# Kernel optimization log

Measured on AMD Instinct MI355X. Metric: run time of the kernel, lower is better.

The kernel has to match this reference:

```python
import jax, jax.numpy as jnp
import numpy as np

B, S, D, H = 2, 2048, 2048, 16
HD = D // H          # head_dim = 128
FF = 8192            # intermediate_size
LN_EPS = 1e-05
BIT_EPS = 1e-05


def _rope_tables(seq_len, head_dim):
    inv_freq = 1.0 / (10000.0 ** (np.arange(0, head_dim, 2, dtype=np.float64) / head_dim))
    ang = np.arange(seq_len, dtype=np.float64)[:, None] * inv_freq[None, :]  # [S, HD/2]
    ang = np.concatenate([ang, ang], axis=-1)  # [S, HD]
    return jnp.asarray(np.cos(ang), jnp.float32), jnp.asarray(np.sin(ang), jnp.float32)


def setup_inputs() -> dict:
    key = jax.random.key(0)
    ks = jax.random.split(key, 9)
    hidden_states = jax.random.normal(ks[0], (B, S, D), jnp.float32)
    # causal additive mask [1, S, S]
    causal = jnp.tril(jnp.ones((S, S), bool))
    attention_mask = jnp.where(causal, 0.0, -1e9)[None].astype(jnp.float32)
    cos, sin = _rope_tables(S, HD)
    w = lambda k, o, i: jax.random.normal(k, (o, i), jnp.float32) * 0.02
    return {
        'hidden_states': hidden_states,
        'attention_mask': attention_mask,
        'cos': cos, 'sin': sin,
        'wq': w(ks[1], D, D), 'wk': w(ks[2], D, D),
        'wv': w(ks[3], D, D), 'wo': w(ks[4], D, D),
        'wg': w(ks[5], FF, D), 'wu': w(ks[6], FF, D), 'wd': w(ks[7], D, FF),
        'ln1_w': jnp.ones((D,), jnp.float32),
        'ln2_w': jnp.ones((D,), jnp.float32),
    }


def bitlinear(x, w):
    # ternarize: clamp(round(w / (mean|w| + eps)), -1, 1); int8 cast in torch
    # breaks grad through the ternary values -> stop_gradient here.
    scale = jnp.mean(jnp.abs(w))
    tern = jax.lax.stop_gradient(jnp.clip(jnp.round(w / (scale + BIT_EPS)), -1.0, 1.0))
    # dequant = ternary * mean|w|, then standard linear (x @ W^T)
    return jnp.einsum('bsi,oi->bso', x, tern * scale)


def rmsnorm(x, w, eps=LN_EPS):
    var = jnp.mean(jnp.square(x.astype(jnp.float32)), axis=-1, keepdims=True)
    return w * (x * jax.lax.rsqrt(var + eps))


def rotate_half(x):
    x1, x2 = jnp.split(x, 2, axis=-1)
    return jnp.concatenate([-x2, x1], axis=-1)


def apply_rope(q, k, cos, sin):
    # q, k: [B, S, D] -> per-head rope -> back to [B, S, D]
    qh = q.reshape(B, S, H, HD)
    kh = k.reshape(B, S, H, HD)
    c = cos[None, :, None, :]
    s = sin[None, :, None, :]
    qe = qh * c + rotate_half(qh) * s
    ke = kh * c + rotate_half(kh) * s
    return qe.reshape(B, S, D), ke.reshape(B, S, D)


def reference(hidden_states, attention_mask, cos, sin,
              wq, wk, wv, wo, wg, wu, wd, ln1_w, ln2_w):
    residual = hidden_states
    # --- attention block ---
    x = rmsnorm(hidden_states, ln1_w)
    q = bitlinear(x, wq)
    k = bitlinear(x, wk)
    v = bitlinear(x, wv)
    q, k = apply_rope(q, k, cos, sin)
    # NOTE: scores over FULL hidden dim (no head split), scaled by sqrt(head_dim),
    # exactly as in the original module.
    scores = jnp.einsum('bsd,btd->bst', q, k) / jnp.sqrt(jnp.float32(HD))
    scores = scores + attention_mask
    probs = jax.nn.softmax(scores, axis=-1)
    attn_out = jnp.einsum('bst,btd->bsd', probs, v)
    attn_out = bitlinear(attn_out, wo)
    h = residual + attn_out
    # --- MLP block ---
    residual = h
    y = rmsnorm(h, ln2_w)
    gated = bitlinear(y, wg) * bitlinear(y, wu)
    out = bitlinear(gated, wd)
    return residual + out
```

## Files before the change

kernel.cpp:

```cpp
#include <hip/hip_runtime.h>
#include <stdint.h>

#define DEV __device__ __forceinline__

typedef __attribute__((ext_vector_type(8))) short short8;
typedef __attribute__((ext_vector_type(8))) __bf16 bf16x8;
typedef __attribute__((ext_vector_type(4))) float f32x4;

DEV unsigned short f2bf(float f) {
  union { float f; unsigned int u; } v; v.f = f;
  unsigned int r = v.u + 0x7fffu + ((v.u >> 16) & 1u);
  return (unsigned short)(r >> 16);
}
DEV float bf2f(unsigned short h) {
  union { unsigned int u; float f; } v; v.u = ((unsigned int)h) << 16;
  return v.f;
}
DEV f32x4 mfma16(short8 a, short8 b, f32x4 c) {
  return __builtin_amdgcn_mfma_f32_16x16x32_bf16(
      __builtin_bit_cast(bf16x8, a), __builtin_bit_cast(bf16x8, b), c, 0, 0, 0);
}
DEV void gload_lds16(const void* g, void* lds) {
  __builtin_amdgcn_global_load_lds(
      (const __attribute__((address_space(1))) void*)g,
      (__attribute__((address_space(3))) void*)lds, 16, 0, 0);
}

struct MArgs {
  const float* src[7];
  unsigned short* dst[7];
  int n[7];
  int sidx[7];
};

__global__ __launch_bounds__(256) void absmean_partial_multi(
    MArgs a, float* __restrict__ partial) {
  const int m = blockIdx.y;
  const float4* w4 = (const float4*)a.src[m];
  const int n4 = a.n[m] >> 2;
  float s = 0.f;
  for (int i = blockIdx.x * 256 + threadIdx.x; i < n4; i += 1024 * 256) {
    float4 v = w4[i];
    s += fabsf(v.x) + fabsf(v.y) + fabsf(v.z) + fabsf(v.w);
  }
#pragma unroll
  for (int mm = 1; mm < 64; mm <<= 1) s += __shfl_xor(s, mm);
  __shared__ float red[4];
  if ((threadIdx.x & 63) == 0) red[threadIdx.x >> 6] = s;
  __syncthreads();
  if (threadIdx.x == 0)
    partial[m * 1024 + blockIdx.x] = red[0] + red[1] + red[2] + red[3];
}

__global__ __launch_bounds__(256) void absmean_final(
    const float* __restrict__ partial, float* __restrict__ scales) {
  __shared__ double red[256];
  const int m = blockIdx.x;
  double s = 0.0;
  for (int i = threadIdx.x; i < 1024; i += 256) s += (double)partial[m * 1024 + i];
  red[threadIdx.x] = s;
  __syncthreads();
  for (int t = 128; t > 0; t >>= 1) {
    if (threadIdx.x < t) red[threadIdx.x] += red[threadIdx.x + t];
    __syncthreads();
  }
  if (threadIdx.x == 0) {
    const long long cnt = (m < 4) ? 4194304ll : 16777216ll;
    scales[m] = (float)(red[0] / (double)cnt);
  }
}

__global__ __launch_bounds__(256) void quantize_multi(
    MArgs a, const float* __restrict__ scales) {
  const int m = blockIdx.y;
  const float sc = scales[a.sidx[m]];
  const float inv = 1.f / (sc + 1e-5f);
  const float4* src = (const float4*)a.src[m];
  ushort4* dst = (ushort4*)a.dst[m];
  const int n4 = a.n[m] >> 2;
  for (int i = blockIdx.x * 256 + threadIdx.x; i < n4; i += 2048 * 256) {
    float4 v = src[i];
    ushort4 o;
    o.x = f2bf(fminf(fmaxf(rintf(v.x * inv), -1.f), 1.f) * sc);
    o.y = f2bf(fminf(fmaxf(rintf(v.y * inv), -1.f), 1.f) * sc);
    o.z = f2bf(fminf(fmaxf(rintf(v.z * inv), -1.f), 1.f) * sc);
    o.w = f2bf(fminf(fmaxf(rintf(v.w * inv), -1.f), 1.f) * sc);
    dst[i] = o;
  }
}

__global__ __launch_bounds__(256) void rmsnorm_k(
    const float* __restrict__ x, const float* __restrict__ wt,
    unsigned short* __restrict__ out) {
  const long long t = blockIdx.x;
  const float* xr = x + t * 2048;
  const int i0 = threadIdx.x * 8;
  float4 a = *(const float4*)(xr + i0);
  float4 b = *(const float4*)(xr + i0 + 4);
  float ss = a.x * a.x + a.y * a.y + a.z * a.z + a.w * a.w +
             b.x * b.x + b.y * b.y + b.z * b.z + b.w * b.w;
#pragma unroll
  for (int m = 1; m < 64; m <<= 1) ss += __shfl_xor(ss, m);
  __shared__ float red[4];
  if ((threadIdx.x & 63) == 0) red[threadIdx.x >> 6] = ss;
  __syncthreads();
  float tot = red[0] + red[1] + red[2] + red[3];
  float rs = rsqrtf(tot * (1.f / 2048.f) + 1e-5f);
  float4 wa = *(const float4*)(wt + i0);
  float4 wb = *(const float4*)(wt + i0 + 4);
  ushort4 o1, o2;
  o1.x = f2bf(a.x * wa.x * rs); o1.y = f2bf(a.y * wa.y * rs);
  o1.z = f2bf(a.z * wa.z * rs); o1.w = f2bf(a.w * wa.w * rs);
  o2.x = f2bf(b.x * wb.x * rs); o2.y = f2bf(b.y * wb.y * rs);
  o2.z = f2bf(b.z * wb.z * rs); o2.w = f2bf(b.w * wb.w * rs);
  *(ushort4*)(out + t * 2048 + i0) = o1;
  *(ushort4*)(out + t * 2048 + i0 + 4) = o2;
}

__global__ __launch_bounds__(256) void rope_k(
    const unsigned short* __restrict__ qkv, const float* __restrict__ cosT,
    const float* __restrict__ sinT, unsigned short* __restrict__ qr,
    unsigned short* __restrict__ kr, unsigned short* __restrict__ vt) {
  const long long gid = (long long)blockIdx.x * 256 + threadIdx.x;
  const int t = (int)(gid >> 10);
  const int r = (int)(gid & 1023);
  const int h = r >> 6, d = r & 63;
  const int s = t & 2047, b = t >> 11;
  const unsigned short* row = qkv + (long long)t * 6144;
  const float c = cosT[s * 128 + d], sn = sinT[s * 128 + d];
  const int col = h * 128 + d;
  const float SC = 0.08838834764831845f;
  float q1 = bf2f(row[col]), q2 = bf2f(row[col + 64]);
  float k1 = bf2f(row[2048 + col]), k2 = bf2f(row[2048 + col + 64]);
  long long ob = (long long)t * 2048 + col;
  qr[ob] = f2bf((q1 * c - q2 * sn) * SC);
  qr[ob + 64] = f2bf((q2 * c + q1 * sn) * SC);
  kr[ob] = f2bf(k1 * c - k2 * sn);
  kr[ob + 64] = f2bf(k2 * c + k1 * sn);
  vt[((long long)b * 2048 + col) * 2048 + s] = row[4096 + col];
  vt[((long long)b * 2048 + col + 64) * 2048 + s] = row[4096 + col + 64];
}

__global__ __launch_bounds__(256) void softmax_causal(
    const float* __restrict__ scores, unsigned short* __restrict__ probs) {
  const int r = blockIdx.x;
  const int s = r & 2047;
  const float* src = scores + (long long)r * 2048;
  unsigned short* dst = probs + (long long)r * 2048;
  const int L = s + 1;
  const int j0 = threadIdx.x * 8;
  float4 a = *(const float4*)(src + j0);
  float4 b = *(const float4*)(src + j0 + 4);
  float v[8] = {a.x, a.y, a.z, a.w, b.x, b.y, b.z, b.w};
  float mx = -1e30f;
#pragma unroll
  for (int i = 0; i < 8; ++i) {
    if (j0 + i >= L) v[i] = -1e30f;
    mx = fmaxf(mx, v[i]);
  }
#pragma unroll
  for (int m = 1; m < 64; m <<= 1) mx = fmaxf(mx, __shfl_xor(mx, m));
  __shared__ float redM[4], redS[4];
  if ((threadIdx.x & 63) == 0) redM[threadIdx.x >> 6] = mx;
  __syncthreads();
  mx = fmaxf(fmaxf(redM[0], redM[1]), fmaxf(redM[2], redM[3]));
  float sum = 0.f;
#pragma unroll
  for (int i = 0; i < 8; ++i) {
    v[i] = (j0 + i < L) ? __expf(v[i] - mx) : 0.f;
    sum += v[i];
  }
#pragma unroll
  for (int m = 1; m < 64; m <<= 1) sum += __shfl_xor(sum, m);
  if ((threadIdx.x & 63) == 0) redS[threadIdx.x >> 6] = sum;
  __syncthreads();
  const float inv = 1.f / (redS[0] + redS[1] + redS[2] + redS[3]);
  ushort4 o1, o2;
  o1.x = f2bf(v[0] * inv); o1.y = f2bf(v[1] * inv);
  o1.z = f2bf(v[2] * inv); o1.w = f2bf(v[3] * inv);
  o2.x = f2bf(v[4] * inv); o2.y = f2bf(v[5] * inv);
  o2.z = f2bf(v[6] * inv); o2.w = f2bf(v[7] * inv);
  *(ushort4*)(dst + j0) = o1;
  *(ushort4*)(dst + j0 + 4) = o2;
}

template <int EPI, int CAUSAL>
__global__ __launch_bounds__(512, 2) void gemm256(
    const unsigned short* __restrict__ A, const unsigned short* __restrict__ Bw,
    void* __restrict__ Cp, const void* __restrict__ Ep,
    int N, int K, int nbx, int kLen, int ngTot,
    long long sAz, long long sBz, long long zCout) {
  __shared__ __align__(16) unsigned short lds[4 * 2 * 8192];
  __shared__ __align__(16) unsigned short ldsDummy[512];
  const int tid = threadIdx.x;
  const int wid = tid >> 6, l = tid & 63;
  const int wr = wid >> 2, wcn = wid & 3;

  const int nwg = gridDim.x;
  const int q8 = nwg >> 3;
  const int lin = (blockIdx.x & 7) * q8 + (blockIdx.x >> 3);
  const int t32 = lin >> 5, r32 = lin & 31;
  const int tpr = nbx >> 3;
  const int tm = t32 / tpr, tn = t32 - tm * tpr;
  const long long m0 = (long long)(tm * 4 + (r32 >> 3)) * 256;
  const long long n0 = (long long)(tn * 8 + (r32 & 7)) * 256;
  if (CAUSAL == 1 && n0 > m0) return;
  const int z = blockIdx.z;
  A += z * sAz;
  Bw += z * sBz;
  const long long kbase = (long long)z * kLen;
  const long long zofs = (long long)z * zCout;
  int ng = ngTot;
  if (CAUSAL == 2) {
    const int lim = (int)((m0 + 256) >> 5);
    ng = lim < ng ? lim : ng;
  }

  const int stRow = (l >> 2);
  const int stCol = (((l & 3) ^ ((l >> 3) & 3))) * 8;
  auto stage = [&](int chunk, int mat) {
    char* base = (char*)lds + (((chunk & 3) * 2 + mat) * 16384);
    const unsigned short* src = mat ? Bw : A;
    const long long rb = mat ? n0 : m0;
    if (chunk < ng) {
      const long long kcol = kbase + (long long)chunk * 32 + stCol;
#pragma unroll
      for (int i = 0; i < 2; ++i) {
        const int row = (wid * 2 + i) * 16 + stRow;
        gload_lds16(&src[(rb + row) * K + kcol], base + (wid * 2 + i) * 1024);
      }
    } else {
#pragma unroll
      for (int i = 0; i < 2; ++i) gload_lds16(&src[rb * K], (char*)ldsDummy);
    }
  };

  const int ar = l & 15;
  const int rj = ((l >> 4) ^ ((l >> 1) & 3)) << 4;

  f32x4 acc[8][4] = {};

  stage(0, 0); stage(0, 1);
  stage(1, 0); stage(1, 1);
  stage(2, 0); stage(2, 1);
  asm volatile("s_waitcnt vmcnt(8)" ::: "memory");
  __builtin_amdgcn_s_barrier();

  for (int c = 0; c < ng; ++c) {
    const int slot = c & 3;
    const char* sA = (const char*)lds + (slot * 2 + 0) * 16384;
    const char* sB = (const char*)lds + (slot * 2 + 1) * 16384;
    short8 af[4], bf[4];
#pragma unroll
    for (int m = 0; m < 4; ++m)
      af[m] = *(const short8*)(sA + (wr * 128 + m * 16 + ar) * 64 + rj);
#pragma unroll
    for (int n = 0; n < 4; ++n)
      bf[n] = *(const short8*)(sB + (wcn * 64 + n * 16 + ar) * 64 + rj);
    stage(c + 3, 0);
    __builtin_amdgcn_s_barrier();
    asm volatile("s_waitcnt lgkmcnt(0)" ::: "memory");
    __builtin_amdgcn_sched_barrier(0);
    __builtin_amdgcn_s_setprio(1);
#pragma unroll
    for (int m = 0; m < 4; ++m)
#pragma unroll
      for (int n = 0; n < 4; ++n) acc[m][n] = mfma16(af[m], bf[n], acc[m][n]);
    __builtin_amdgcn_s_setprio(0);
    __builtin_amdgcn_s_barrier();
#pragma unroll
    for (int m = 0; m < 4; ++m)
      af[m] = *(const short8*)(sA + (wr * 128 + (m + 4) * 16 + ar) * 64 + rj);
    stage(c + 3, 1);
    __builtin_amdgcn_s_barrier();
    asm volatile("s_waitcnt lgkmcnt(0)" ::: "memory");
    __builtin_amdgcn_sched_barrier(0);
    __builtin_amdgcn_s_setprio(1);
#pragma unroll
    for (int m = 0; m < 4; ++m)
#pragma unroll
      for (int n = 0; n < 4; ++n)
        acc[m + 4][n] = mfma16(af[m], bf[n], acc[m + 4][n]);
    __builtin_amdgcn_s_setprio(0);
    asm volatile("s_waitcnt vmcnt(8)" ::: "memory");
    __builtin_amdgcn_s_barrier();
  }
  asm volatile("s_waitcnt vmcnt(0)" ::: "memory");
  __builtin_amdgcn_s_barrier();

  const int orow = (l >> 4) * 4, ocol = l & 15;
#pragma unroll
  for (int m = 0; m < 8; ++m)
#pragma unroll
    for (int n = 0; n < 4; ++n)
#pragma unroll
      for (int r = 0; r < 4; ++r) {
        const long long gr = m0 + wr * 128 + m * 16 + orow + r;
        const long long gc = n0 + wcn * 64 + n * 16 + ocol;
        const long long idx = zofs + gr * N + gc;
        const float v = acc[m][n][r];
        if (EPI == 0) {
          ((unsigned short*)Cp)[idx] = f2bf(v);
        } else if (EPI == 2) {
          ((unsigned short*)Cp)[idx] = f2bf(bf2f(((const unsigned short*)Ep)[idx]) * v);
        } else {
          ((float*)Cp)[idx] = v;
        }
      }
}

__global__ __launch_bounds__(256) void combine2(
    const float* __restrict__ ep, const float* __restrict__ p,
    float* __restrict__ out, long long n4) {
  const float4* e4 = (const float4*)ep;
  const float4* p4 = (const float4*)p;
  float4* o4 = (float4*)out;
  for (long long i = blockIdx.x * 256 + threadIdx.x; i < n4; i += 2048 * 256) {
    float4 a = e4[i], b = p4[i], c = p4[i + n4];
    float4 o;
    o.x = a.x + b.x + c.x; o.y = a.y + b.y + c.y;
    o.z = a.z + b.z + c.z; o.w = a.w + b.w + c.w;
    o4[i] = o;
  }
}

extern "C" void kernel_launch(void* const* d_in, const int* in_sizes, int n_in,
                              void* d_out, int out_size, void* d_ws, size_t ws_size,
                              hipStream_t stream) {
  (void)in_sizes; (void)n_in; (void)out_size; (void)ws_size;
  const float* hidden = (const float*)d_in[0];
  const float* cosT = (const float*)d_in[2];
  const float* sinT = (const float*)d_in[3];
  const float* wq = (const float*)d_in[4];
  const float* wk = (const float*)d_in[5];
  const float* wv = (const float*)d_in[6];
  const float* wo = (const float*)d_in[7];
  const float* wg = (const float*)d_in[8];
  const float* wu = (const float*)d_in[9];
  const float* wd = (const float*)d_in[10];
  const float* ln1 = (const float*)d_in[11];
  const float* ln2 = (const float*)d_in[12];

  const size_t MB = 1ull << 20;
  char* ws = (char*)d_ws;
  unsigned short* xn    = (unsigned short*)(ws + 0);
  unsigned short* wqkvq = (unsigned short*)(ws + 16 * MB);
  unsigned short* qkv   = (unsigned short*)(ws + 40 * MB);
  unsigned short* qrb   = (unsigned short*)(ws + 88 * MB);
  unsigned short* krb   = (unsigned short*)(ws + 104 * MB);
  unsigned short* vtb   = (unsigned short*)(ws + 120 * MB);
  float*          scoresB = (float*)(ws + 0);
  unsigned short* probsB  = (unsigned short*)(ws + 40 * MB);
  float*          part   = (float*)(ws + 0);
  unsigned short* wgq   = (unsigned short*)(ws + 0);
  unsigned short* wuq   = (unsigned short*)(ws + 32 * MB);
  unsigned short* gbuf  = (unsigned short*)(ws + 64 * MB);
  unsigned short* attnb = (unsigned short*)(ws + 136 * MB);
  unsigned short* woq   = (unsigned short*)(ws + 152 * MB);
  float*          hbuf  = (float*)(ws + 160 * MB);
  unsigned short* ybuf  = (unsigned short*)(ws + 192 * MB);
  unsigned short* gated = (unsigned short*)(ws + 208 * MB);
  unsigned short* wdq   = (unsigned short*)(ws + 272 * MB);
  float* wspart         = (float*)(ws + 304 * MB);
  float* scales         = (float*)(ws + 304 * MB + 32768);

  MArgs am;
  am.src[0] = wq; am.src[1] = wk; am.src[2] = wv; am.src[3] = wo;
  am.src[4] = wg; am.src[5] = wu; am.src[6] = wd;
  am.n[0] = am.n[1] = am.n[2] = am.n[3] = 4194304;
  am.n[4] = am.n[5] = am.n[6] = 16777216;
  for (int i = 0; i < 7; ++i) { am.dst[i] = nullptr; am.sidx[i] = i; }
  absmean_partial_multi<<<dim3(1024, 7), 256, 0, stream>>>(am, wspart);
  absmean_final<<<7, 256, 0, stream>>>(wspart, scales);

  MArgs qe;
  qe.src[0] = wq; qe.dst[0] = wqkvq;            qe.n[0] = 4194304;  qe.sidx[0] = 0;
  qe.src[1] = wk; qe.dst[1] = wqkvq + 4194304;  qe.n[1] = 4194304;  qe.sidx[1] = 1;
  qe.src[2] = wv; qe.dst[2] = wqkvq + 8388608;  qe.n[2] = 4194304;  qe.sidx[2] = 2;
  qe.src[3] = wo; qe.dst[3] = woq;              qe.n[3] = 4194304;  qe.sidx[3] = 3;
  qe.src[4] = wd; qe.dst[4] = wdq;              qe.n[4] = 16777216; qe.sidx[4] = 6;
  qe.src[5] = wq; qe.dst[5] = nullptr; qe.n[5] = 0; qe.sidx[5] = 0;
  qe.src[6] = wq; qe.dst[6] = nullptr; qe.n[6] = 0; qe.sidx[6] = 0;
  quantize_multi<<<dim3(2048, 5), 256, 0, stream>>>(qe, scales);

  rmsnorm_k<<<4096, 256, 0, stream>>>(hidden, ln1, xn);

  gemm256<0, 0><<<dim3(384, 1, 1), 512, 0, stream>>>(
      xn, wqkvq, qkv, nullptr, 6144, 2048, 24, 2048, 64, 0, 0, 0);

  rope_k<<<16384, 256, 0, stream>>>(qkv, cosT, sinT, qrb, krb, vtb);

  gemm256<4, 1><<<dim3(64, 1, 2), 512, 0, stream>>>(
      qrb, krb, scoresB, nullptr, 2048, 2048, 8, 0, 64, 4194304, 4194304, 4194304);
  softmax_causal<<<4096, 256, 0, stream>>>(scoresB, probsB);
  gemm256<0, 2><<<dim3(64, 1, 2), 512, 0, stream>>>(
      probsB, vtb, attnb, nullptr, 2048, 2048, 8, 0, 64, 4194304, 4194304, 4194304);

  gemm256<4, 0><<<dim3(128, 1, 2), 512, 0, stream>>>(
      attnb, woq, part, nullptr, 2048, 2048, 8, 1024, 32, 0, 0, 8388608);
  combine2<<<2048, 256, 0, stream>>>(hidden, part, hbuf, 2097152);

  MArgs ql;
  ql.src[0] = wg; ql.dst[0] = wgq; ql.n[0] = 16777216; ql.sidx[0] = 4;
  ql.src[1] = wu; ql.dst[1] = wuq; ql.n[1] = 16777216; ql.sidx[1] = 5;
  for (int i = 2; i < 7; ++i) { ql.src[i] = wg; ql.dst[i] = nullptr; ql.n[i] = 0; ql.sidx[i] = 0; }
  quantize_multi<<<dim3(2048, 2), 256, 0, stream>>>(ql, scales);

  rmsnorm_k<<<4096, 256, 0, stream>>>(hbuf, ln2, ybuf);

  gemm256<0, 0><<<dim3(512, 1, 1), 512, 0, stream>>>(
      ybuf, wgq, gbuf, nullptr, 8192, 2048, 32, 2048, 64, 0, 0, 0);
  gemm256<2, 0><<<dim3(512, 1, 1), 512, 0, stream>>>(
      ybuf, wuq, gated, gbuf, 8192, 2048, 32, 2048, 64, 0, 0, 0);

  gemm256<4, 0><<<dim3(128, 1, 2), 512, 0, stream>>>(
      gated, wdq, part, nullptr, 2048, 8192, 8, 4096, 128, 0, 0, 8388608);
  combine2<<<2048, 256, 0, stream>>>(hbuf, part, (float*)d_out, 2097152);
}
```

Baseline: 898.4 us.

## Software-pipeline LDS fragment reads across chunks and merge A/B staging

Restructures the GEMM main loop so the next chunk's A(0-3) and B fragments are read from LDS while the second half of the current chunk's MFMAs runs, using double-buffered register fragments and a loop unrolled by two. A and B global-to-LDS loads for a chunk are issued together, and the per-chunk barriers drop from four to one. The aim is to hide LDS read latency behind MFMA work and cut barrier stalls. In exchange it uses more registers, and the unroll-by-two loop assumes ng is even; otherwise the extra iteration computes with stale data.

After: 825.7 us. 1.09x faster.

```diff
diff --git a/kernel.cpp b/kernel.cpp
--- a/kernel.cpp
+++ b/kernel.cpp
@@ -218,72 +218,82 @@
 
   const int stRow = (l >> 2);
   const int stCol = (((l & 3) ^ ((l >> 3) & 3))) * 8;
-  auto stage = [&](int chunk, int mat) {
-    char* base = (char*)lds + (((chunk & 3) * 2 + mat) * 16384);
-    const unsigned short* src = mat ? Bw : A;
-    const long long rb = mat ? n0 : m0;
+  auto stage = [&](int chunk) {
     if (chunk < ng) {
+      char* base = (char*)lds + ((chunk & 3) * 2) * 16384;
       const long long kcol = kbase + (long long)chunk * 32 + stCol;
 #pragma unroll
       for (int i = 0; i < 2; ++i) {
         const int row = (wid * 2 + i) * 16 + stRow;
-        gload_lds16(&src[(rb + row) * K + kcol], base + (wid * 2 + i) * 1024);
+        gload_lds16(&A[(m0 + row) * K + kcol], base + (wid * 2 + i) * 1024);
+        gload_lds16(&Bw[(n0 + row) * K + kcol],
+                    base + 16384 + (wid * 2 + i) * 1024);
       }
     } else {
 #pragma unroll
-      for (int i = 0; i < 2; ++i) gload_lds16(&src[rb * K], (char*)ldsDummy);
+      for (int i = 0; i < 4; ++i) gload_lds16(&A[m0 * K], (char*)ldsDummy);
     }
   };
 
   const int ar = l & 15;
   const int rj = ((l >> 4) ^ ((l >> 1) & 3)) << 4;
 
+  auto readA03 = [&](int slot, short8 (&a)[4]) {
+    const char* sA = (const char*)lds + (slot * 2) * 16384;
+#pragma unroll
+    for (int m = 0; m < 4; ++m)
+      a[m] = *(const short8*)(sA + (wr * 128 + m * 16 + ar) * 64 + rj);
+  };
+  auto readA47 = [&](int slot, short8 (&a)[4]) {
+    const char* sA = (const char*)lds + (slot * 2) * 16384;
+#pragma unroll
+    for (int m = 0; m < 4; ++m)
+      a[m] = *(const short8*)(sA + (wr * 128 + (m + 4) * 16 + ar) * 64 + rj);
+  };
+  auto readB = [&](int slot, short8 (&b)[4]) {
+    const char* sB = (const char*)lds + (slot * 2 + 1) * 16384;
+#pragma unroll
+    for (int n = 0; n < 4; ++n)
+      b[n] = *(const short8*)(sB + (wcn * 64 + n * 16 + ar) * 64 + rj);
+  };
+
   f32x4 acc[8][4] = {};
-
-  stage(0, 0); stage(0, 1);
-  stage(1, 0); stage(1, 1);
-  stage(2, 0); stage(2, 1);
+  short8 aX[4], bX[4], aY[4], bY[4], a47[4];
+
+  stage(0); stage(1); stage(2);
   asm volatile("s_waitcnt vmcnt(8)" ::: "memory");
   __builtin_amdgcn_s_barrier();
-
-  for (int c = 0; c < ng; ++c) {
+  readA03(0, aX);
+  readB(0, bX);
+
+  auto chunkBody = [&](int c, short8 (&cur03)[4], short8 (&curB)[4],
+                       short8 (&nxt03)[4], short8 (&nxtB)[4]) {
     const int slot = c & 3;
-    const char* sA = (const char*)lds + (slot * 2 + 0) * 16384;
-    const char* sB = (const char*)lds + (slot * 2 + 1) * 16384;
-    short8 af[4], bf[4];
+    readA47(slot, a47);
+    stage(c + 3);
+    __builtin_amdgcn_s_setprio(1);
 #pragma unroll
     for (int m = 0; m < 4; ++m)
-      af[m] = *(const short8*)(sA + (wr * 128 + m * 16 + ar) * 64 + rj);
-#pragma unroll
-    for (int n = 0; n < 4; ++n)
-      bf[n] = *(const short8*)(sB + (wcn * 64 + n * 16 + ar) * 64 + rj);
-    stage(c + 3, 0);
-    __builtin_amdgcn_s_barrier();
-    asm volatile("s_waitcnt lgkmcnt(0)" ::: "memory");
-    __builtin_amdgcn_sched_barrier(0);
-    __builtin_amdgcn_s_setprio(1);
-#pragma unroll
-    for (int m = 0; m < 4; ++m)
-#pragma unroll
-      for (int n = 0; n < 4; ++n) acc[m][n] = mfma16(af[m], bf[n], acc[m][n]);
-    __builtin_amdgcn_s_setprio(0);
-    __builtin_amdgcn_s_barrier();
-#pragma unroll
-    for (int m = 0; m < 4; ++m)
-      af[m] = *(const short8*)(sA + (wr * 128 + (m + 4) * 16 + ar) * 64 + rj);
-    stage(c + 3, 1);
-    __builtin_amdgcn_s_barrier();
-    asm volatile("s_waitcnt lgkmcnt(0)" ::: "memory");
-    __builtin_amdgcn_sched_barrier(0);
-    __builtin_amdgcn_s_setprio(1);
-#pragma unroll
-    for (int m = 0; m < 4; ++m)
 #pragma unroll
       for (int n = 0; n < 4; ++n)
-        acc[m + 4][n] = mfma16(af[m], bf[n], acc[m + 4][n]);
+        acc[m][n] = mfma16(cur03[m], curB[n], acc[m][n]);
     __builtin_amdgcn_s_setprio(0);
     asm volatile("s_waitcnt vmcnt(8)" ::: "memory");
     __builtin_amdgcn_s_barrier();
+    readA03((c + 1) & 3, nxt03);
+    readB((c + 1) & 3, nxtB);
+    __builtin_amdgcn_s_setprio(1);
+#pragma unroll
+    for (int m = 0; m < 4; ++m)
+#pragma unroll
+      for (int n = 0; n < 4; ++n)
+        acc[m + 4][n] = mfma16(a47[m], curB[n], acc[m + 4][n]);
+    __builtin_amdgcn_s_setprio(0);
+  };
+
+  for (int c = 0; c < ng; c += 2) {
+    chunkBody(c, aX, bX, aY, bY);
+    chunkBody(c + 1, aY, bY, aX, bX);
   }
   asm volatile("s_waitcnt vmcnt(0)" ::: "memory");
   __builtin_amdgcn_s_barrier();
```
